# Kernel optimization log

Hardware: AMD Instinct MI355X
Metric: run time of the kernel (lower is better)

Reference implementation:

```python
import jax, jax.numpy as jnp
import numpy as np

CORR = 5          # corr_size (patch_size)
UP = 2            # upsample_param
CH = [512, 1024, 512, 256, 256, 256]
SZ = [64, 32, 16, 8, 4, 2]   # pyramid spatial sizes; UP*2**i upsamples all to 128
B = 2
P = CORR * CORR

def upsample_nearest(x, f):
    # nn.Upsample(scale_factor=f, mode='nearest') for integer f
    return jnp.repeat(jnp.repeat(x, f, axis=2), f, axis=3)

def correlate(f1, f2):
    # spatial_correlation_sample: kernel=1, patch=CORR, stride=1, padding=0, dilation_patch=1
    # out[b, pi*CORR+pj, y, x] = sum_c f1[b,c,y,x] * f2[b,c,y+pi-r,x+pj-r] (zeros out of range)
    r = CORR // 2
    b, c, h, w = f1.shape
    f2p = jnp.pad(f2, ((0, 0), (0, 0), (r, r), (r, r)))
    outs = []
    for pi in range(CORR):
        for pj in range(CORR):
            sh = jax.lax.dynamic_slice(f2p, (0, 0, pi, pj), (b, c, h, w))
            outs.append(jnp.sum(f1 * sh, axis=1))
    return jnp.stack(outs, axis=1)  # [B, P, h, w]

def avgpool(x):
    # AvgPool2d(kernel_size=3, stride=2, padding=1), count_include_pad=True (torch default)
    s = jax.lax.reduce_window(x, 0.0, jax.lax.add, (1, 1, 3, 3), (1, 1, 2, 2), ((0, 0), (0, 0), (1, 1), (1, 1)))
    return s / 9.0

def conv3x3(x, w, b):
    y = jax.lax.conv_general_dilated(x, w, (1, 1), ((1, 1), (1, 1)), dimension_numbers=("NCHW", "OIHW", "NCHW"))
    return y + b[None, :, None, None]

def level_step(feat1, feat2, h_pre, c_pre, w, b, lvl):
    f = UP * (2 ** lvl)
    u1 = upsample_nearest(feat1, f)
    u2 = upsample_nearest(feat2, f)
    corr = jax.nn.leaky_relu(correlate(u1, u2), 0.01)
    # int(log2(up_W / feat_W)) pools; this is <= 6 so only avg_pooling1 is ever used
    for _ in range(int(np.log2(u1.shape[3] // feat1.shape[3]))):
        corr = avgpool(corr)
    gates = conv3x3(jnp.concatenate([corr, h_pre], axis=1), w, b)
    i = jax.nn.sigmoid(gates[:, :P])
    fg = jax.nn.sigmoid(gates[:, P:2 * P])
    o = jax.nn.sigmoid(gates[:, 2 * P:3 * P])
    g = jnp.tanh(gates[:, 3 * P:])
    c_next = fg * c_pre + i * g
    h_next = o * jnp.tanh(c_next)
    return h_next, c_next

def setup_inputs():
    keys = jax.random.split(jax.random.key(0), 40)
    d = {}
    k = 0
    for i in range(6):
        d[f"x{i}"] = jax.random.normal(keys[k], (B, CH[i], SZ[i], SZ[i]), jnp.float32); k += 1
        d[f"xp{i}"] = jax.random.normal(keys[k], (B, CH[i], SZ[i], SZ[i]), jnp.float32); k += 1
        d[f"h{i}"] = jax.random.normal(keys[k], (B, P, SZ[i], SZ[i]), jnp.float32); k += 1
        d[f"c{i}"] = jax.random.normal(keys[k], (B, P, SZ[i], SZ[i]), jnp.float32); k += 1
    for i in range(6):
        d[f"W{i}"] = jax.random.normal(keys[k], (4 * P, 2 * P, 3, 3), jnp.float32) * 0.05; k += 1
        d[f"b{i}"] = jnp.zeros((4 * P,), jnp.float32)
    return d

def reference(x0, x1, x2, x3, x4, x5, xp0, xp1, xp2, xp3, xp4, xp5,
              h0, h1, h2, h3, h4, h5, c0, c1, c2, c3, c4, c5,
              W0, W1, W2, W3, W4, W5, b0, b1, b2, b3, b4, b5):
    xs = [x0, x1, x2, x3, x4, x5]
    xps = [xp0, xp1, xp2, xp3, xp4, xp5]
    hs = [h0, h1, h2, h3, h4, h5]
    cs = [c0, c1, c2, c3, c4, c5]
    Ws = [W0, W1, W2, W3, W4, W5]
    bs = [b0, b1, b2, b3, b4, b5]
    outs = []
    for lvl in range(6):
        h_next, c_next = level_step(xs[lvl], xps[lvl], hs[lvl], cs[lvl], Ws[lvl], bs[lvl], lvl)
        outs.extend([h_next, c_next])
    return tuple(outs)
```

## Files before the change

### kernel.cpp

```cpp
#include <hip/hip_runtime.h>

#define NB 2
#define PP 25
#define NLVL 6

struct Params {
  const float* x1[NLVL];
  const float* x2[NLVL];
  const float* h[NLVL];
  const float* c[NLVL];
  const float* W[NLVL];
  const float* bias[NLVL];
  float* Dpart[NLVL];
  float* D[NLVL];
  float* pooled[NLVL];
  float* WT[NLVL];
  float* hout[NLVL];
  float* cout[NLVL];
};

__device__ __forceinline__ float lrelu(float v) { return v > 0.f ? v : 0.01f * v; }

__global__ __launch_bounds__(256) void repack_kernel(Params pr) {
  const int lvl = blockIdx.y;
  const float* W = pr.W[lvl];
  float* WT = pr.WT[lvl];
  for (int i = blockIdx.x * 256 + threadIdx.x; i < 100 * 450; i += gridDim.x * 256) {
    const int oc = i / 450;
    const int r = i - oc * 450;
    WT[r * 100 + oc] = W[i];
  }
}

__global__ __launch_bounds__(256) void dcorr_kernel(Params pr) {
  static const int SZt[6] = {64, 32, 16, 8, 4, 2};
  static const int CHt[6] = {512, 1024, 512, 256, 256, 256};
  static const int NCH[6] = {32, 64, 4, 1, 1, 1};
  const int lvl = blockIdx.y;
  const int S = SZt[lvl], C = CHt[lvl], nch = NCH[lvl];
  const int bid = blockIdx.x;
  const int tid = threadIdx.x;
  const size_t nlev = (size_t)NB * S * S * 9;

  if (lvl <= 1) {
    int b, y, chunk, xq;
    if (lvl == 0) {
      chunk = bid & 31;
      const int rest = bid >> 5;
      const int yt = rest & 3;
      b = rest >> 2;
      xq = tid & 15;
      y = yt * 16 + (tid >> 4);
    } else {
      if (bid >= 128) return;
      chunk = bid & 63;
      b = bid >> 6;
      xq = tid & 7;
      y = tid >> 3;
    }
    const int xb0 = xq << 2;
    const int c0 = chunk * 16;

    const float* f1b = pr.x1[lvl] + (((size_t)b * C + c0) * S + y) * S + xb0;
    const float* f2b = pr.x2[lvl] + ((size_t)b * C + c0) * S * S;

    float acc[9][4];
#pragma unroll
    for (int jj = 0; jj < 9; ++jj)
#pragma unroll
      for (int j = 0; j < 4; ++j) acc[jj][j] = 0.f;

#pragma unroll 4
    for (int t = 0; t < 16; ++t) {
      const float4 f1 = *(const float4*)(f1b + (size_t)t * S * S);
      const float f1a[4] = {f1.x, f1.y, f1.z, f1.w};
      const float* p2 = f2b + (size_t)t * S * S;
#pragma unroll
      for (int dy = 0; dy < 3; ++dy) {
        const int yy = y + dy - 1;
        const bool yok = (yy >= 0) && (yy < S);
        const float* prow = p2 + (size_t)yy * S;
        float4 m;
        float lm, rm;
        if (yok) {
          m = *(const float4*)(prow + xb0);
          lm = (xb0 > 0) ? prow[xb0 - 1] : 0.f;
          rm = (xb0 + 4 < S) ? prow[xb0 + 4] : 0.f;
        } else {
          m = make_float4(0.f, 0.f, 0.f, 0.f);
          lm = 0.f;
          rm = 0.f;
        }
        const float wl[4] = {lm, m.x, m.y, m.z};
        const float wc[4] = {m.x, m.y, m.z, m.w};
        const float wr[4] = {m.y, m.z, m.w, rm};
#pragma unroll
        for (int j = 0; j < 4; ++j) {
          acc[dy * 3 + 0][j] = fmaf(f1a[j], wl[j], acc[dy * 3 + 0][j]);
          acc[dy * 3 + 1][j] = fmaf(f1a[j], wc[j], acc[dy * 3 + 1][j]);
          acc[dy * 3 + 2][j] = fmaf(f1a[j], wr[j], acc[dy * 3 + 2][j]);
        }
      }
    }

    float4 buf4[9];
    float* buf = (float*)buf4;
#pragma unroll
    for (int j = 0; j < 4; ++j)
#pragma unroll
      for (int jj = 0; jj < 9; ++jj) buf[j * 9 + jj] = acc[jj][j];
    float* out = pr.Dpart[lvl] + (size_t)chunk * nlev +
                 ((size_t)(b * S + y) * S + xb0) * 9;
#pragma unroll
    for (int v = 0; v < 9; ++v) ((float4*)out)[v] = buf4[v];
    return;
  }

  const int rows = NB * S;
  if (bid >= rows * nch) return;
  const int row = bid / nch;
  const int chunk = bid - row * nch;
  const int b = row / S, yb = row - b * S;
  float* part = pr.Dpart[lvl] + (size_t)chunk * nlev;

  __shared__ float red[9216];

  if (S >= 16) {
    const int lgq = 2;
    const int xqn = S >> 2;
    const int cgn = 256 >> lgq;
    const int xq = tid & (xqn - 1);
    const int cg = tid >> lgq;
    const int chpc = C / nch;
    const int cpt = chpc / cgn;
    const int xb0 = xq << 2;

    const float* f1b = pr.x1[lvl] + (size_t)b * C * S * S + (size_t)yb * S + xb0;
    const float* f2b = pr.x2[lvl] + (size_t)b * C * S * S;

    float acc[9][4];
#pragma unroll
    for (int jj = 0; jj < 9; ++jj)
#pragma unroll
      for (int j = 0; j < 4; ++j) acc[jj][j] = 0.f;

    const int c0 = chunk * chpc + cg;
    for (int t = 0; t < cpt; ++t) {
      const int cc = c0 + t * cgn;
      const float4 f1 = *(const float4*)(f1b + (size_t)cc * S * S);
      const float f1a[4] = {f1.x, f1.y, f1.z, f1.w};
      const float* p2 = f2b + (size_t)cc * S * S;
#pragma unroll
      for (int dy = 0; dy < 3; ++dy) {
        const int yy = yb + dy - 1;
        if (yy < 0 || yy >= S) continue;
        const float* prow = p2 + (size_t)yy * S;
        const float4 m = *(const float4*)(prow + xb0);
        const float lm = (xb0 > 0) ? prow[xb0 - 1] : 0.f;
        const float rm = (xb0 + 4 < S) ? prow[xb0 + 4] : 0.f;
        const float wl[4] = {lm, m.x, m.y, m.z};
        const float wc[4] = {m.x, m.y, m.z, m.w};
        const float wr[4] = {m.y, m.z, m.w, rm};
#pragma unroll
        for (int j = 0; j < 4; ++j) {
          acc[dy * 3 + 0][j] = fmaf(f1a[j], wl[j], acc[dy * 3 + 0][j]);
          acc[dy * 3 + 1][j] = fmaf(f1a[j], wc[j], acc[dy * 3 + 1][j]);
          acc[dy * 3 + 2][j] = fmaf(f1a[j], wr[j], acc[dy * 3 + 2][j]);
        }
      }
    }

    const int n = S * 9;
#pragma unroll
    for (int jj = 0; jj < 9; ++jj)
#pragma unroll
      for (int j = 0; j < 4; ++j)
        red[cg * n + (xb0 + j) * 9 + jj] = acc[jj][j];
    __syncthreads();
    for (int g = cgn >> 1; g >= 1; g >>= 1) {
      for (int i = tid; i < g * n; i += 256) {
        const int c = i / n, e = i - c * n;
        red[c * n + e] += red[(c + g) * n + e];
      }
      __syncthreads();
    }
    float* out = part + (size_t)(b * S + yb) * S * 9;
    for (int i = tid; i < n; i += 256) out[i] = red[i];
  } else {
    const int lg = (S == 8) ? 3 : ((S == 4) ? 2 : 1);
    const int xb = tid & (S - 1), cg = tid >> lg;
    const int NG = 256 >> lg;
    const int cpt = C / NG;

    const float* f1base = pr.x1[lvl] + (size_t)b * C * S * S + (size_t)yb * S + xb;
    const float* f2base = pr.x2[lvl] + (size_t)b * C * S * S;

    float acc[9];
#pragma unroll
    for (int j = 0; j < 9; ++j) acc[j] = 0.f;

    for (int t = 0; t < cpt; ++t) {
      const int cc = cg + t * NG;
      const float f1 = f1base[(size_t)cc * S * S];
      const float* p2 = f2base + (size_t)cc * S * S;
#pragma unroll
      for (int dy = 0; dy < 3; ++dy) {
        const int yy = yb + dy - 1;
        if (yy < 0 || yy >= S) continue;
        const float* prow = p2 + yy * S;
#pragma unroll
        for (int dx = 0; dx < 3; ++dx) {
          const int xx = xb + dx - 1;
          const float v = (xx >= 0 && xx < S) ? prow[xx] : 0.f;
          acc[dy * 3 + dx] += f1 * v;
        }
      }
    }

#pragma unroll
    for (int j = 0; j < 9; ++j) red[tid * 9 + j] = acc[j];
    __syncthreads();
    for (int g = NG >> 1; g >= 1; g >>= 1) {
      if (cg < g) {
#pragma unroll
        for (int j = 0; j < 9; ++j) red[tid * 9 + j] += red[(tid + g * S) * 9 + j];
      }
      __syncthreads();
    }
    if (cg == 0) {
      float* Dp = part + ((size_t)(b * S + yb) * S + xb) * 9;
#pragma unroll
      for (int j = 0; j < 9; ++j) Dp[j] = red[tid * 9 + j];
    }
  }
}

__global__ __launch_bounds__(256) void dreduce_kernel(Params pr) {
  static const int SZt[6] = {64, 32, 16, 8, 4, 2};
  static const int NCH[6] = {32, 64, 4, 1, 1, 1};
  const int lvl = blockIdx.y;
  const int S = SZt[lvl], nch = NCH[lvl];
  const int n4 = (NB * S * S * 9) >> 2;
  const int i4 = blockIdx.x * 256 + threadIdx.x;
  if (i4 >= n4) return;
  const float4* part = (const float4*)pr.Dpart[lvl];
  float4 s = make_float4(0.f, 0.f, 0.f, 0.f);
  if (nch >= 8) {
    for (int c0 = 0; c0 < nch; c0 += 8) {
      float4 v[8];
#pragma unroll
      for (int k = 0; k < 8; ++k) v[k] = part[(size_t)(c0 + k) * n4 + i4];
#pragma unroll
      for (int k = 0; k < 4; ++k) {
        v[k].x += v[k + 4].x; v[k].y += v[k + 4].y;
        v[k].z += v[k + 4].z; v[k].w += v[k + 4].w;
      }
#pragma unroll
      for (int k = 0; k < 2; ++k) {
        v[k].x += v[k + 2].x; v[k].y += v[k + 2].y;
        v[k].z += v[k + 2].z; v[k].w += v[k + 2].w;
      }
      s.x += v[0].x + v[1].x; s.y += v[0].y + v[1].y;
      s.z += v[0].z + v[1].z; s.w += v[0].w + v[1].w;
    }
  } else {
    for (int c = 0; c < nch; ++c) {
      const float4 v = part[(size_t)c * n4 + i4];
      s.x += v.x; s.y += v.y; s.z += v.z; s.w += v.w;
    }
  }
  float4 o;
  o.x = lrelu(s.x); o.y = lrelu(s.y); o.z = lrelu(s.z); o.w = lrelu(s.w);
  ((float4*)pr.D[lvl])[i4] = o;
}

__global__ __launch_bounds__(256) void pool_kernel(Params pr) {
  static const int SZt[6] = {64, 32, 16, 8, 4, 2};
  static const int NYC[6] = {8, 4, 2, 1, 1, 1};
  static const int LGS[6] = {6, 5, 4, 3, 2, 1};
  const int lvl = blockIdx.y;
  const int S = SZt[lvl], k = lvl + 1, f = 1 << k, nyc = NYC[lvl], lgS = LGS[lvl];
  const int nyo = S / nyc;
  const int bid = blockIdx.x;
  if (bid >= 50 * nyc) return;
  const int yc = bid / 50;
  const int bp = bid - yc * 50;
  const int b = bp / 25, p = bp - (bp / 25) * 25;
  const int dpy = p / 5 - 2, dpx = p - (p / 5) * 5 - 2;
  const int tid = threadIdx.x;
  const int yo0 = yc * nyo;

  __shared__ float ckb[2][130], clb[2][66];
  __shared__ float Dl[5184];
  __shared__ float tmp[1024];

  if (tid == 0) { ckb[0][0] = 1.f; clb[0][0] = 1.f; }
  __syncthreads();
  int rj = 0, cur = 0;
  for (int j = 0; j < k; ++j) {
    const int half = 1 << j, rn = 2 * half - 1;
    float cknew = 0.f, clnew = 0.f;
    if (tid <= 2 * rn) {
      const int t = tid - rn;
#pragma unroll
      for (int e = -1; e <= 1; ++e) {
        const int u = t + e * half;
        if (u >= -rj && u <= rj) cknew += ckb[cur][u + rj];
      }
      cknew *= (1.f / 3.f);
    }
    if (tid < 2 * half) {
      const int y = tid;
      float s = (y < half) ? clb[cur][y] : 0.f;
      const int u = y - half;
      if (u >= -rj && u <= rj) s += ckb[cur][u + rj];
      clnew = s * (1.f / 3.f);
    }
    __syncthreads();
    if (tid <= 2 * rn) ckb[cur ^ 1][tid] = cknew;
    if (tid < 2 * half) clb[cur ^ 1][tid] = clnew;
    __syncthreads();
    cur ^= 1;
    rj = rn;
  }
  const float* ck = ckb[cur];
  const float* cl = clb[cur];

  const int yb0 = (yo0 > 0) ? yo0 - 1 : 0;
  const int nyb = (yo0 + nyo - 1) - yb0 + 1;
  const float* Dg = pr.D[lvl] + (size_t)b * S * S * 9 + (size_t)yb0 * S * 9;
  const int nload = nyb * S * 9;
  for (int i = tid; i < nload; i += 256) Dl[i] = Dg[i];
  __syncthreads();

  for (int item = tid; item < nyo * 128; item += 256) {
    const int yol = item >> 7, x = item & 127;
    const int yo = yo0 + yol;
    const int xb = x >> k, tx = x & (f - 1);
    const int txp = tx + dpx;
    const int dxi = (txp < 0) ? 0 : ((txp >= f) ? 2 : 1);
    float sum = 0.f;
    if (yo == 0) {
      for (int y = 0; y < f; ++y) {
        const int typ = y + dpy;
        const int dyi = (typ < 0) ? 0 : ((typ >= f) ? 2 : 1);
        sum += cl[y] * Dl[((0 - yb0) * S + xb) * 9 + dyi * 3 + dxi];
      }
    } else {
      const int ylo = yo * f - (f - 1);
      for (int t = 0; t < 2 * f - 1; ++t) {
        const int y = ylo + t;
        const int yb = y >> k, ty = y & (f - 1);
        const int typ = ty + dpy;
        const int dyi = (typ < 0) ? 0 : ((typ >= f) ? 2 : 1);
        sum += ck[t] * Dl[((yb - yb0) * S + xb) * 9 + dyi * 3 + dxi];
      }
    }
    tmp[yol * 128 + x] = sum;
  }
  __syncthreads();

  float* out = pr.pooled[lvl] + (size_t)(b * PP + p) * S * S;
  for (int item = tid; item < nyo * S; item += 256) {
    const int yol = item >> lgS, xo = item & (S - 1);
    float sum = 0.f;
    if (xo == 0) {
      for (int x = 0; x < f; ++x) sum += cl[x] * tmp[yol * 128 + x];
    } else {
      const int xlo = xo * f - (f - 1);
      for (int t = 0; t < 2 * f - 1; ++t) sum += ck[t] * tmp[yol * 128 + xlo + t];
    }
    out[(size_t)(yo0 + yol) * S + xo] = sum;
  }
}

__global__ __launch_bounds__(256) void conv_kernel(Params pr) {
  static const int SZt[6] = {64, 32, 16, 8, 4, 2};
  static const int XTt[6] = {16, 16, 16, 8, 4, 2};
  static const int NXGt[6] = {2, 2, 2, 1, 1, 1};
  const int lvl = blockIdx.y;
  const int S = SZt[lvl], xtile = XTt[lvl], nxg = NXGt[lvl];
  const int nxt = S / xtile;
  const int nblk = NB * S * nxt;
  const int bid = blockIdx.x;
  if (bid >= nblk) return;
  const int b = bid / (S * nxt);
  const int rem = bid - b * (S * nxt);
  const int y = rem / nxt;
  const int xt = rem - y * nxt;
  const int xb0 = xt * xtile;
  const int tid = threadIdx.x;
  const int icc = tid >> 6;
  const int sub = tid & 63;
  const int nact = 25 * nxg;

  __shared__ float lds[7232];

  {
    const float* pooled = pr.pooled[lvl] + (size_t)b * PP * S * S;
    const float* hin = pr.h[lvl] + (size_t)b * PP * S * S;
    for (int i = tid; i < 150 * 20; i += 256) {
      const int r = i / 20, j = i - r * 20;
      const int ky = r / 50, ic = r - ky * 50;
      const int yy = y + ky - 1;
      const int x = xb0 + j - 1;
      float v = 0.f;
      if (yy >= 0 && yy < S && x >= 0 && x < S && j < xtile + 2)
        v = (ic < PP) ? pooled[((size_t)ic * S + yy) * S + x]
                      : hin[((size_t)(ic - PP) * S + yy) * S + x];
      lds[r * 20 + j] = v;
    }
  }
  __syncthreads();

  float acc[4][8];
#pragma unroll
  for (int q = 0; q < 4; ++q)
#pragma unroll
    for (int xx = 0; xx < 8; ++xx) acc[q][xx] = 0.f;

  if (sub < nact) {
    const int xg = sub / 25;
    const int p = sub - xg * 25;
    const int xoff = xg * 8;
    const int ic0 = (icc * 50) >> 2;
    const int ic1 = ((icc + 1) * 50) >> 2;
    const float* wbase = pr.WT[lvl] + p;

    float w[4][9], wn[4][9];
#pragma unroll
    for (int q = 0; q < 4; ++q)
#pragma unroll
      for (int t = 0; t < 9; ++t) w[q][t] = wbase[((size_t)ic0 * 9 + t) * 100 + q * 25];

    for (int ic = ic0; ic < ic1; ++ic) {
      const bool pre = (ic + 1 < ic1);
      if (pre) {
        const float* wq = wbase + (size_t)(ic + 1) * 900;
#pragma unroll
        for (int q = 0; q < 4; ++q)
#pragma unroll
          for (int t = 0; t < 9; ++t) wn[q][t] = wq[t * 100 + q * 25];
      }
#pragma unroll
      for (int ky = 0; ky < 3; ++ky) {
        const float4* rp = (const float4*)(lds + (ky * 50 + ic) * 20 + xoff);
        const float4 A = rp[0], Bv = rp[1], Cv = rp[2];
        const float sg[12] = {A.x, A.y, A.z, A.w, Bv.x, Bv.y, Bv.z, Bv.w,
                              Cv.x, Cv.y, Cv.z, Cv.w};
#pragma unroll
        for (int q = 0; q < 4; ++q) {
          const float w0 = w[q][ky * 3], w1 = w[q][ky * 3 + 1], w2 = w[q][ky * 3 + 2];
#pragma unroll
          for (int xx = 0; xx < 8; ++xx)
            acc[q][xx] = fmaf(w0, sg[xx], fmaf(w1, sg[xx + 1], fmaf(w2, sg[xx + 2], acc[q][xx])));
        }
      }
      if (pre) {
#pragma unroll
        for (int q = 0; q < 4; ++q)
#pragma unroll
          for (int t = 0; t < 9; ++t) w[q][t] = wn[q][t];
      }
    }
  }
  __syncthreads();

  if (sub < nact) {
    float* slot = lds + (icc * 50 + sub) * 36;
#pragma unroll
    for (int q = 0; q < 4; ++q) {
      ((float4*)slot)[q * 2] = make_float4(acc[q][0], acc[q][1], acc[q][2], acc[q][3]);
      ((float4*)slot)[q * 2 + 1] = make_float4(acc[q][4], acc[q][5], acc[q][6], acc[q][7]);
    }
  }
  __syncthreads();

  if (tid < nact) {
    const int xg2 = tid / 25;
    const int p2 = tid - xg2 * 25;
    const int xoff2 = xg2 * 8;

    float g4[4][8];
#pragma unroll
    for (int q = 0; q < 4; ++q)
#pragma unroll
      for (int xx = 0; xx < 8; ++xx) {
        float s = 0.f;
#pragma unroll
        for (int k2 = 0; k2 < 4; ++k2) s += lds[(k2 * 50 + tid) * 36 + q * 8 + xx];
        g4[q][xx] = s;
      }

    const float bi = pr.bias[lvl][p2];
    const float bf = pr.bias[lvl][p2 + 25];
    const float bo = pr.bias[lvl][p2 + 50];
    const float bg = pr.bias[lvl][p2 + 75];
    const size_t base = ((size_t)(b * PP + p2) * S + y) * S + xb0 + xoff2;
    const float* cin = pr.c[lvl] + base;
    float* ho = pr.hout[lvl] + base;
    float* co = pr.cout[lvl] + base;

    float cp[8], hn[8], cn[8];
    if (S >= 8) {
      const float4 c0 = ((const float4*)cin)[0];
      const float4 c1 = ((const float4*)cin)[1];
      cp[0] = c0.x; cp[1] = c0.y; cp[2] = c0.z; cp[3] = c0.w;
      cp[4] = c1.x; cp[5] = c1.y; cp[6] = c1.z; cp[7] = c1.w;
    } else {
#pragma unroll
      for (int xx = 0; xx < 8; ++xx) cp[xx] = (xx < S) ? cin[xx] : 0.f;
    }
#pragma unroll
    for (int xx = 0; xx < 8; ++xx) {
      const float gi = g4[0][xx] + bi;
      const float gf = g4[1][xx] + bf;
      const float go = g4[2][xx] + bo;
      const float gg = g4[3][xx] + bg;
      const float i_ = 1.f / (1.f + __expf(-gi));
      const float f_ = 1.f / (1.f + __expf(-gf));
      const float o_ = 1.f / (1.f + __expf(-go));
      const float g_ = 1.f - 2.f / (__expf(2.f * gg) + 1.f);
      const float c_ = f_ * cp[xx] + i_ * g_;
      const float t2 = 1.f - 2.f / (__expf(2.f * c_) + 1.f);
      cn[xx] = c_;
      hn[xx] = o_ * t2;
    }
    if (S >= 8) {
      ((float4*)ho)[0] = make_float4(hn[0], hn[1], hn[2], hn[3]);
      ((float4*)ho)[1] = make_float4(hn[4], hn[5], hn[6], hn[7]);
      ((float4*)co)[0] = make_float4(cn[0], cn[1], cn[2], cn[3]);
      ((float4*)co)[1] = make_float4(cn[4], cn[5], cn[6], cn[7]);
    } else {
#pragma unroll
      for (int xx = 0; xx < 8; ++xx)
        if (xx < S) { ho[xx] = hn[xx]; co[xx] = cn[xx]; }
    }
  }
}

extern "C" void kernel_launch(void* const* d_in, const int* in_sizes, int n_in,
                              void* d_out, int out_size, void* d_ws, size_t ws_size,
                              hipStream_t stream) {
  static const int SZ[NLVL] = {64, 32, 16, 8, 4, 2};
  static const int NCH[NLVL] = {32, 64, 4, 1, 1, 1};

  Params pr;
  float* ws = (float*)d_ws;
  size_t off = 0;
  for (int l = 0; l < NLVL; ++l) {
    pr.Dpart[l] = ws + off;
    off += (size_t)NCH[l] * NB * SZ[l] * SZ[l] * 9;
  }
  for (int l = 0; l < NLVL; ++l) { pr.D[l] = ws + off; off += (size_t)NB * SZ[l] * SZ[l] * 9; }
  for (int l = 0; l < NLVL; ++l) { pr.pooled[l] = ws + off; off += (size_t)NB * PP * SZ[l] * SZ[l]; }
  for (int l = 0; l < NLVL; ++l) { pr.WT[l] = ws + off; off += 100 * 450; }

  float* out = (float*)d_out;
  size_t ooff = 0;
  for (int l = 0; l < NLVL; ++l) {
    pr.hout[l] = out + ooff; ooff += (size_t)NB * PP * SZ[l] * SZ[l];
    pr.cout[l] = out + ooff; ooff += (size_t)NB * PP * SZ[l] * SZ[l];
  }

  for (int l = 0; l < NLVL; ++l) {
    pr.x1[l] = (const float*)d_in[4 * l + 0];
    pr.x2[l] = (const float*)d_in[4 * l + 1];
    pr.h[l]  = (const float*)d_in[4 * l + 2];
    pr.c[l]  = (const float*)d_in[4 * l + 3];
    pr.W[l]    = (const float*)d_in[24 + 2 * l];
    pr.bias[l] = (const float*)d_in[25 + 2 * l];
  }

  repack_kernel<<<dim3(45, NLVL), 256, 0, stream>>>(pr);
  dcorr_kernel<<<dim3(256, NLVL), 256, 0, stream>>>(pr);
  dreduce_kernel<<<dim3(72, NLVL), 256, 0, stream>>>(pr);
  pool_kernel<<<dim3(400, NLVL), 256, 0, stream>>>(pr);
  conv_kernel<<<dim3(512, NLVL), 256, 0, stream>>>(pr);
}
```

Baseline: 231.4 us.

## Repack conv weights per output pixel and split input channels over 8 groups

The weight repack now stores, for each gate position p, all 36 weights (4 gates x 9 taps) of each input channel contiguously, so the conv inner loop loads them with nine float4 reads instead of strided scalar loads. The explicit double-buffered weight prefetch is dropped. The conv kernel moves to 512 threads with 8 input-channel groups instead of 4, which doubles the LDS partial-sum area. The final reduction over groups uses vectorized float4 LDS reads. This aims to cut global load count and add parallelism per block, at the cost of more LDS, a larger block and a deeper cross-group reduction.

Result: slower. 276.5 us (+19.5%).

```diff
diff --git a/kernel.cpp b/kernel.cpp
--- a/kernel.cpp
+++ b/kernel.cpp
@@ -14,7 +14,7 @@
   float* Dpart[NLVL];
   float* D[NLVL];
   float* pooled[NLVL];
-  float* WT[NLVL];
+  float* WTP[NLVL];
   float* hout[NLVL];
   float* cout[NLVL];
 };
@@ -24,11 +24,15 @@
 __global__ __launch_bounds__(256) void repack_kernel(Params pr) {
   const int lvl = blockIdx.y;
   const float* W = pr.W[lvl];
-  float* WT = pr.WT[lvl];
+  float* WTP = pr.WTP[lvl];
   for (int i = blockIdx.x * 256 + threadIdx.x; i < 100 * 450; i += gridDim.x * 256) {
     const int oc = i / 450;
-    const int r = i - oc * 450;
-    WT[r * 100 + oc] = W[i];
+    const int rem = i - oc * 450;
+    const int ic = rem / 9;
+    const int t = rem - ic * 9;
+    const int q = oc / 25;
+    const int p = oc - q * 25;
+    WTP[((size_t)p * 50 + ic) * 36 + q * 9 + t] = W[i];
   }
 }
 
@@ -374,7 +378,7 @@
   }
 }
 
-__global__ __launch_bounds__(256) void conv_kernel(Params pr) {
+__global__ __launch_bounds__(512, 4) void conv_kernel(Params pr) {
   static const int SZt[6] = {64, 32, 16, 8, 4, 2};
   static const int XTt[6] = {16, 16, 16, 8, 4, 2};
   static const int NXGt[6] = {2, 2, 2, 1, 1, 1};
@@ -394,12 +398,12 @@
   const int sub = tid & 63;
   const int nact = 25 * nxg;
 
-  __shared__ float lds[7232];
+  __shared__ float lds[14400];
 
   {
     const float* pooled = pr.pooled[lvl] + (size_t)b * PP * S * S;
     const float* hin = pr.h[lvl] + (size_t)b * PP * S * S;
-    for (int i = tid; i < 150 * 20; i += 256) {
+    for (int i = tid; i < 150 * 20; i += 512) {
       const int r = i / 20, j = i - r * 20;
       const int ky = r / 50, ic = r - ky * 50;
       const int yy = y + ky - 1;
@@ -423,25 +427,16 @@
     const int xg = sub / 25;
     const int p = sub - xg * 25;
     const int xoff = xg * 8;
-    const int ic0 = (icc * 50) >> 2;
-    const int ic1 = ((icc + 1) * 50) >> 2;
-    const float* wbase = pr.WT[lvl] + p;
-
-    float w[4][9], wn[4][9];
-#pragma unroll
-    for (int q = 0; q < 4; ++q)
-#pragma unroll
-      for (int t = 0; t < 9; ++t) w[q][t] = wbase[((size_t)ic0 * 9 + t) * 100 + q * 25];
+    const int ic0 = (icc * 50) >> 3;
+    const int ic1 = ((icc + 1) * 50) >> 3;
+    const float* wtp = pr.WTP[lvl] + (size_t)p * 50 * 36;
 
     for (int ic = ic0; ic < ic1; ++ic) {
-      const bool pre = (ic + 1 < ic1);
-      if (pre) {
-        const float* wq = wbase + (size_t)(ic + 1) * 900;
-#pragma unroll
-        for (int q = 0; q < 4; ++q)
-#pragma unroll
-          for (int t = 0; t < 9; ++t) wn[q][t] = wq[t * 100 + q * 25];
-      }
+      float w[36];
+      const float4* wr = (const float4*)(wtp + (size_t)ic * 36);
+#pragma unroll
+      for (int v = 0; v < 9; ++v) ((float4*)w)[v] = wr[v];
+
 #pragma unroll
       for (int ky = 0; ky < 3; ++ky) {
         const float4* rp = (const float4*)(lds + (ky * 50 + ic) * 20 + xoff);
@@ -450,17 +445,13 @@
                               Cv.x, Cv.y, Cv.z, Cv.w};
 #pragma unroll
         for (int q = 0; q < 4; ++q) {
-          const float w0 = w[q][ky * 3], w1 = w[q][ky * 3 + 1], w2 = w[q][ky * 3 + 2];
+          const float w0 = w[q * 9 + ky * 3];
+          const float w1 = w[q * 9 + ky * 3 + 1];
+          const float w2 = w[q * 9 + ky * 3 + 2];
 #pragma unroll
           for (int xx = 0; xx < 8; ++xx)
             acc[q][xx] = fmaf(w0, sg[xx], fmaf(w1, sg[xx + 1], fmaf(w2, sg[xx + 2], acc[q][xx])));
         }
-      }
-      if (pre) {
-#pragma unroll
-        for (int q = 0; q < 4; ++q)
-#pragma unroll
-          for (int t = 0; t < 9; ++t) w[q][t] = wn[q][t];
       }
     }
   }
@@ -485,12 +476,18 @@
 #pragma unroll
     for (int q = 0; q < 4; ++q)
 #pragma unroll
-      for (int xx = 0; xx < 8; ++xx) {
-        float s = 0.f;
-#pragma unroll
-        for (int k2 = 0; k2 < 4; ++k2) s += lds[(k2 * 50 + tid) * 36 + q * 8 + xx];
-        g4[q][xx] = s;
-      }
+      for (int xx = 0; xx < 8; ++xx) g4[q][xx] = 0.f;
+#pragma unroll
+    for (int k2 = 0; k2 < 8; ++k2) {
+      const float* slot = lds + (k2 * 50 + tid) * 36;
+#pragma unroll
+      for (int q = 0; q < 4; ++q) {
+        const float4 a = ((const float4*)slot)[q * 2];
+        const float4 b2 = ((const float4*)slot)[q * 2 + 1];
+        g4[q][0] += a.x;  g4[q][1] += a.y;  g4[q][2] += a.z;  g4[q][3] += a.w;
+        g4[q][4] += b2.x; g4[q][5] += b2.y; g4[q][6] += b2.z; g4[q][7] += b2.w;
+      }
+    }
 
     const float bi = pr.bias[lvl][p2];
     const float bf = pr.bias[lvl][p2 + 25];
@@ -554,7 +551,7 @@
   }
   for (int l = 0; l < NLVL; ++l) { pr.D[l] = ws + off; off += (size_t)NB * SZ[l] * SZ[l] * 9; }
   for (int l = 0; l < NLVL; ++l) { pr.pooled[l] = ws + off; off += (size_t)NB * PP * SZ[l] * SZ[l]; }
-  for (int l = 0; l < NLVL; ++l) { pr.WT[l] = ws + off; off += 100 * 450; }
+  for (int l = 0; l < NLVL; ++l) { pr.WTP[l] = ws + off; off += 25 * 50 * 36; }
 
   float* out = (float*)d_out;
   size_t ooff = 0;
@@ -576,5 +573,5 @@
   dcorr_kernel<<<dim3(256, NLVL), 256, 0, stream>>>(pr);
   dreduce_kernel<<<dim3(72, NLVL), 256, 0, stream>>>(pr);
   pool_kernel<<<dim3(400, NLVL), 256, 0, stream>>>(pr);
-  conv_kernel<<<dim3(512, NLVL), 256, 0, stream>>>(pr);
+  conv_kernel<<<dim3(512, NLVL), 512, 0, stream>>>(pr);
 }
```
